# Performance work log

Hardware: AMD Instinct MI355X
Metric: run time of the kernel (lower is better)

The kernel has to match this reference:

```python
import jax, jax.numpy as jnp
import numpy as np

L_TAU = 0.8  # membrane leak/decay factor (l_tau in the torch module)
T, B, IN, H = 100, 256, 1024, 1024


def setup_inputs() -> dict:
    key = jax.random.key(0)
    k_x, k_w1, k_b1, k_w2, k_b2 = jax.random.split(key, 5)
    x = jax.random.normal(k_x, (T, B, IN), dtype=jnp.float32)
    W1 = jax.random.normal(k_w1, (H, IN), dtype=jnp.float32) / np.sqrt(IN)
    b1 = jax.random.normal(k_b1, (H,), dtype=jnp.float32) * 0.1 - 0.5
    W2 = jax.random.normal(k_w2, (H, H), dtype=jnp.float32) / np.sqrt(H)
    b2 = jax.random.normal(k_b2, (H,), dtype=jnp.float32) * 0.1 - 0.5
    return {"x": x, "W1": W1, "b1": b1, "W2": W2, "b2": b2}


def reference(x, W1, b1, W2, b2):
    """Two stacked SNU (spiking neural unit) layers scanned over T timesteps.

    Per layer (hard / non-soft SNU):
      u_t = W x_t + l_tau * s_{t-1} * (1 - y_{t-1})   # leaky membrane with reset-on-spike
      s_t = relu(u_t)                                  # membrane potential
      y_t = heaviside(s_t + b)                         # spike output
    Returns (spikes_l1 [T,B,H], mem_l1 [T,B,H], mem_l2 [T,B,H]) matching the
    torch forward's (spikes_, mem1_out, mem2_out).
    """
    dt = x.dtype
    Bsz = x.shape[1]
    H1 = W1.shape[0]
    H2 = W2.shape[0]

    def step(carry, x_t):
        s1, y1, s2, y2 = carry
        u1 = x_t @ W1.T + L_TAU * s1 * (1.0 - y1)     # [B, H1]
        s1n = jax.nn.relu(u1)
        y1n = (s1n + b1 > 0.0).astype(dt)
        u2 = y1n @ W2.T + L_TAU * s2 * (1.0 - y2)     # [B, H2]
        s2n = jax.nn.relu(u2)
        y2n = (s2n + b2 > 0.0).astype(dt)
        return (s1n, y1n, s2n, y2n), (y1n, s1n, s2n)

    init = (
        jnp.zeros((Bsz, H1), dt), jnp.zeros((Bsz, H1), dt),
        jnp.zeros((Bsz, H2), dt), jnp.zeros((Bsz, H2), dt),
    )
    _, (spikes, mem1, mem2) = jax.lax.scan(step, init, x)
    return spikes, mem1, mem2
```

## Files before the change

### kernel.cpp

```cpp
#include <hip/hip_runtime.h>


#define TILE 128
#define BK 32
#define NTILE (512 / BK)

typedef const __attribute__((address_space(1))) void* gptr_t;
typedef __attribute__((address_space(3))) void* sptr_t;

template<int ADD>
__global__ __launch_bounds__(256) void gemm_nt_swz(
    const float* __restrict__ A,
    const float* __restrict__ B,
    float* __restrict__ C,
    int N, int M, int K, int kbase)
{
#pragma clang fp contract(off)
    __shared__ float As[TILE * BK];
    __shared__ float Bs[TILE * BK];

    const int tid  = threadIdx.x;
    const int w    = tid >> 6;
    const int lane = tid & 63;
    const int tx   = lane & 7;
    const int ty   = lane >> 3;
    const int wr   = w >> 1;
    const int wc   = w & 1;
    const int row0 = wr * 64 + ty * 8;
    const int col0 = wc * 64 + tx * 8;

    const int n0 = blockIdx.x * TILE;
    const int m0 = blockIdx.y * TILE;

    const int lr8 = lane >> 3;
    const int lc  = lane & 7;

    float acc[8][8];
#pragma unroll
    for (int i = 0; i < 8; ++i)
#pragma unroll
        for (int j = 0; j < 8; ++j) acc[i][j] = 0.f;

    for (int kt = 0; kt < NTILE; ++kt) {
        const int k0 = kbase + kt * BK;
        __syncthreads();
#pragma unroll
        for (int is = 0; is < 4; ++is) {
            const int rb   = w * 4 + is;
            const int srow = rb * 8 + lr8;
            const int sc   = lc ^ (rb & 7);
            const float* ga = A + (size_t)(n0 + srow) * K + k0 + sc * 4;
            const float* gb = B + (size_t)(m0 + srow) * K + k0 + sc * 4;
            __builtin_amdgcn_global_load_lds((gptr_t)ga, (sptr_t)(As + rb * 8 * BK), 16, 0, 0);
            __builtin_amdgcn_global_load_lds((gptr_t)gb, (sptr_t)(Bs + rb * 8 * BK), 16, 0, 0);
        }
        __syncthreads();

#pragma unroll
        for (int c = 0; c < 8; ++c) {
            float4 bf[8];
#pragma unroll
            for (int j = 0; j < 8; ++j)
                bf[j] = *(const float4*)&Bs[(col0 + j) * BK + ((c ^ tx) << 2)];
#pragma unroll
            for (int i = 0; i < 8; ++i) {
                float4 af = *(const float4*)&As[(row0 + i) * BK + ((c ^ ty) << 2)];
#pragma unroll
                for (int j = 0; j < 8; ++j) {
                    acc[i][j] = __builtin_fmaf(af.x, bf[j].x, acc[i][j]);
                    acc[i][j] = __builtin_fmaf(af.y, bf[j].y, acc[i][j]);
                    acc[i][j] = __builtin_fmaf(af.z, bf[j].z, acc[i][j]);
                    acc[i][j] = __builtin_fmaf(af.w, bf[j].w, acc[i][j]);
                }
            }
        }
    }

#pragma unroll
    for (int i = 0; i < 8; ++i) {
        size_t row = (size_t)(n0 + row0 + i);
        float* Cp = C + row * M + m0 + col0;
        if (ADD) {
            float4 o0 = *(float4*)Cp;
            float4 o1 = *(float4*)(Cp + 4);
            o0.x = o0.x + acc[i][0]; o0.y = o0.y + acc[i][1];
            o0.z = o0.z + acc[i][2]; o0.w = o0.w + acc[i][3];
            o1.x = o1.x + acc[i][4]; o1.y = o1.y + acc[i][5];
            o1.z = o1.z + acc[i][6]; o1.w = o1.w + acc[i][7];
            *(float4*)Cp       = o0;
            *(float4*)(Cp + 4) = o1;
        } else {
            float4 o0 = {acc[i][0], acc[i][1], acc[i][2], acc[i][3]};
            float4 o1 = {acc[i][4], acc[i][5], acc[i][6], acc[i][7]};
            *(float4*)Cp       = o0;
            *(float4*)(Cp + 4) = o1;
        }
    }
}

__global__ __launch_bounds__(256) void scan_l1v(
    const float* __restrict__ Z, const float* __restrict__ bias,
    float* __restrict__ spikes, float* __restrict__ mem, int T, int BH)
{
#pragma clang fp contract(off)
    const int BH4 = BH >> 2;
    int i4 = blockIdx.x * blockDim.x + threadIdx.x;
    if (i4 >= BH4) return;
    const float4* Zv = (const float4*)Z;
    float4* spv  = (float4*)spikes;
    float4* memv = (float4*)mem;
    const float4 bb = *(const float4*)&bias[(i4 << 2) & 1023];

    float4 s = {0.f,0.f,0.f,0.f}, y = {0.f,0.f,0.f,0.f};
    float4 z = Zv[i4];
    for (int t = 0; t < T; ++t) {
        size_t idx = (size_t)t * BH4 + i4;
        float4 zn;
        if (t + 1 < T) zn = Zv[idx + BH4]; else zn = make_float4(0.f,0.f,0.f,0.f);
        float u;
        u = z.x + (0.8f * s.x) * (1.0f - y.x); s.x = fmaxf(u, 0.f); y.x = ((s.x + bb.x) > 0.f) ? 1.f : 0.f;
        u = z.y + (0.8f * s.y) * (1.0f - y.y); s.y = fmaxf(u, 0.f); y.y = ((s.y + bb.y) > 0.f) ? 1.f : 0.f;
        u = z.z + (0.8f * s.z) * (1.0f - y.z); s.z = fmaxf(u, 0.f); y.z = ((s.z + bb.z) > 0.f) ? 1.f : 0.f;
        u = z.w + (0.8f * s.w) * (1.0f - y.w); s.w = fmaxf(u, 0.f); y.w = ((s.w + bb.w) > 0.f) ? 1.f : 0.f;
        spv[idx]  = y;
        memv[idx] = s;
        z = zn;
    }
}

__global__ __launch_bounds__(256) void scan_l2v(
    float* __restrict__ Z, const float* __restrict__ bias, int T, int BH)
{
#pragma clang fp contract(off)
    const int BH4 = BH >> 2;
    int i4 = blockIdx.x * blockDim.x + threadIdx.x;
    if (i4 >= BH4) return;
    float4* Zv = (float4*)Z;
    const float4 bb = *(const float4*)&bias[(i4 << 2) & 1023];

    float4 s = {0.f,0.f,0.f,0.f}, y = {0.f,0.f,0.f,0.f};
    float4 z = Zv[i4];
    for (int t = 0; t < T; ++t) {
        size_t idx = (size_t)t * BH4 + i4;
        float4 zn;
        if (t + 1 < T) zn = Zv[idx + BH4]; else zn = make_float4(0.f,0.f,0.f,0.f);
        float u;
        u = z.x + (0.8f * s.x) * (1.0f - y.x); s.x = fmaxf(u, 0.f); y.x = ((s.x + bb.x) > 0.f) ? 1.f : 0.f;
        u = z.y + (0.8f * s.y) * (1.0f - y.y); s.y = fmaxf(u, 0.f); y.y = ((s.y + bb.y) > 0.f) ? 1.f : 0.f;
        u = z.z + (0.8f * s.z) * (1.0f - y.z); s.z = fmaxf(u, 0.f); y.z = ((s.z + bb.z) > 0.f) ? 1.f : 0.f;
        u = z.w + (0.8f * s.w) * (1.0f - y.w); s.w = fmaxf(u, 0.f); y.w = ((s.w + bb.w) > 0.f) ? 1.f : 0.f;
        Zv[idx] = s;
        z = zn;
    }
}

extern "C" void kernel_launch(void* const* d_in, const int* in_sizes, int n_in,
                              void* d_out, int out_size, void* d_ws, size_t ws_size,
                              hipStream_t stream)
{
    (void)in_sizes; (void)n_in; (void)out_size; (void)d_ws; (void)ws_size;

    const float* x  = (const float*)d_in[0];
    const float* W1 = (const float*)d_in[1];
    const float* b1 = (const float*)d_in[2];
    const float* W2 = (const float*)d_in[3];
    const float* b2 = (const float*)d_in[4];
    float* out = (float*)d_out;

    const int T = 100, Bsz = 256, IN = 1024, H = 1024;
    const int N  = T * Bsz;
    const int BH = Bsz * H;
    const size_t TBH = (size_t)T * BH;

    float* spikes = out;
    float* mem1   = out + TBH;
    float* zbuf   = out + 2 * TBH;

    dim3 ggrid(N / TILE, H / TILE);
    dim3 gblk(256);
    dim3 sgrid((BH / 4) / 256);
    dim3 sblk(256);

    gemm_nt_swz<0><<<ggrid, gblk, 0, stream>>>(x, W1, zbuf, N, H, IN, 0);
    gemm_nt_swz<1><<<ggrid, gblk, 0, stream>>>(x, W1, zbuf, N, H, IN, 512);
    scan_l1v<<<sgrid, sblk, 0, stream>>>(zbuf, b1, spikes, mem1, T, BH);
    gemm_nt_swz<0><<<ggrid, gblk, 0, stream>>>(spikes, W2, zbuf, N, H, H, 0);
    gemm_nt_swz<1><<<ggrid, gblk, 0, stream>>>(spikes, W2, zbuf, N, H, H, 512);
    scan_l2v<<<sgrid, sblk, 0, stream>>>(zbuf, b2, T, BH);
}
```

Measured before the change: 1.489 ms.

## Double-buffer GEMM LDS tiles and remap blocks for L2-friendly grouping

```diff
diff --git a/kernel.cpp b/kernel.cpp
--- a/kernel.cpp
+++ b/kernel.cpp
@@ -8,16 +8,53 @@
 typedef const __attribute__((address_space(1))) void* gptr_t;
 typedef __attribute__((address_space(3))) void* sptr_t;
 
+#define STAGE(ktv, AS, BS) do {                                               \
+    const int k0s = kbase + (ktv) * BK;                                       \
+    _Pragma("unroll")                                                         \
+    for (int is = 0; is < 4; ++is) {                                          \
+        const int rb   = w * 4 + is;                                          \
+        const int srow = rb * 8 + lr8;                                        \
+        const int sc   = lc ^ (rb & 7);                                       \
+        const float* ga = A + (size_t)(n0 + srow) * K + k0s + sc * 4;         \
+        const float* gb = B + (size_t)(m0 + srow) * K + k0s + sc * 4;         \
+        __builtin_amdgcn_global_load_lds((gptr_t)ga, (sptr_t)((AS) + rb * 8 * BK), 16, 0, 0); \
+        __builtin_amdgcn_global_load_lds((gptr_t)gb, (sptr_t)((BS) + rb * 8 * BK), 16, 0, 0); \
+    }                                                                         \
+} while (0)
+
+#define COMPUTE(AS, BS) do {                                                  \
+    _Pragma("unroll")                                                         \
+    for (int c = 0; c < 8; ++c) {                                             \
+        float4 bf[8];                                                         \
+        _Pragma("unroll")                                                     \
+        for (int j = 0; j < 8; ++j)                                           \
+            bf[j] = *(const float4*)&(BS)[(col0 + j) * BK + ((c ^ tx) << 2)]; \
+        _Pragma("unroll")                                                     \
+        for (int i = 0; i < 8; ++i) {                                         \
+            float4 af = *(const float4*)&(AS)[(row0 + i) * BK + ((c ^ ty) << 2)]; \
+            _Pragma("unroll")                                                 \
+            for (int j = 0; j < 8; ++j) {                                     \
+                acc[i][j] = __builtin_fmaf(af.x, bf[j].x, acc[i][j]);         \
+                acc[i][j] = __builtin_fmaf(af.y, bf[j].y, acc[i][j]);         \
+                acc[i][j] = __builtin_fmaf(af.z, bf[j].z, acc[i][j]);         \
+                acc[i][j] = __builtin_fmaf(af.w, bf[j].w, acc[i][j]);         \
+            }                                                                 \
+        }                                                                     \
+    }                                                                         \
+} while (0)
+
 template<int ADD>
-__global__ __launch_bounds__(256) void gemm_nt_swz(
+__global__ __launch_bounds__(256) void gemm_nt_db2(
     const float* __restrict__ A,
     const float* __restrict__ B,
     float* __restrict__ C,
     int N, int M, int K, int kbase)
 {
 #pragma clang fp contract(off)
-    __shared__ float As[TILE * BK];
-    __shared__ float Bs[TILE * BK];
+    __shared__ float As0[TILE * BK];
+    __shared__ float Bs0[TILE * BK];
+    __shared__ float As1[TILE * BK];
+    __shared__ float Bs1[TILE * BK];
 
     const int tid  = threadIdx.x;
     const int w    = tid >> 6;
@@ -29,8 +66,11 @@
     const int row0 = wr * 64 + ty * 8;
     const int col0 = wc * 64 + tx * 8;
 
-    const int n0 = blockIdx.x * TILE;
-    const int m0 = blockIdx.y * TILE;
+    const int id = blockIdx.x;
+    const int bx = (id & 7) | ((id >> 6) << 3);
+    const int by = (id >> 3) & 7;
+    const int n0 = bx * TILE;
+    const int m0 = by * TILE;
 
     const int lr8 = lane >> 3;
     const int lc  = lane & 7;
@@ -41,39 +81,16 @@
 #pragma unroll
         for (int j = 0; j < 8; ++j) acc[i][j] = 0.f;
 
-    for (int kt = 0; kt < NTILE; ++kt) {
-        const int k0 = kbase + kt * BK;
+    STAGE(0, As0, Bs0);
+    __syncthreads();
+
+    for (int kt = 0; kt < NTILE; kt += 2) {
+        if (kt + 1 < NTILE) STAGE(kt + 1, As1, Bs1);
+        COMPUTE(As0, Bs0);
         __syncthreads();
-#pragma unroll
-        for (int is = 0; is < 4; ++is) {
-            const int rb   = w * 4 + is;
-            const int srow = rb * 8 + lr8;
-            const int sc   = lc ^ (rb & 7);
-            const float* ga = A + (size_t)(n0 + srow) * K + k0 + sc * 4;
-            const float* gb = B + (size_t)(m0 + srow) * K + k0 + sc * 4;
-            __builtin_amdgcn_global_load_lds((gptr_t)ga, (sptr_t)(As + rb * 8 * BK), 16, 0, 0);
-            __builtin_amdgcn_global_load_lds((gptr_t)gb, (sptr_t)(Bs + rb * 8 * BK), 16, 0, 0);
-        }
+        if (kt + 2 < NTILE) STAGE(kt + 2, As0, Bs0);
+        COMPUTE(As1, Bs1);
         __syncthreads();
-
-#pragma unroll
-        for (int c = 0; c < 8; ++c) {
-            float4 bf[8];
-#pragma unroll
-            for (int j = 0; j < 8; ++j)
-                bf[j] = *(const float4*)&Bs[(col0 + j) * BK + ((c ^ tx) << 2)];
-#pragma unroll
-            for (int i = 0; i < 8; ++i) {
-                float4 af = *(const float4*)&As[(row0 + i) * BK + ((c ^ ty) << 2)];
-#pragma unroll
-                for (int j = 0; j < 8; ++j) {
-                    acc[i][j] = __builtin_fmaf(af.x, bf[j].x, acc[i][j]);
-                    acc[i][j] = __builtin_fmaf(af.y, bf[j].y, acc[i][j]);
-                    acc[i][j] = __builtin_fmaf(af.z, bf[j].z, acc[i][j]);
-                    acc[i][j] = __builtin_fmaf(af.w, bf[j].w, acc[i][j]);
-                }
-            }
-        }
     }
 
 #pragma unroll
@@ -176,15 +193,15 @@
     float* mem1   = out + TBH;
     float* zbuf   = out + 2 * TBH;
 
-    dim3 ggrid(N / TILE, H / TILE);
+    dim3 ggrid((N / TILE) * (H / TILE));
     dim3 gblk(256);
     dim3 sgrid((BH / 4) / 256);
     dim3 sblk(256);
 
-    gemm_nt_swz<0><<<ggrid, gblk, 0, stream>>>(x, W1, zbuf, N, H, IN, 0);
-    gemm_nt_swz<1><<<ggrid, gblk, 0, stream>>>(x, W1, zbuf, N, H, IN, 512);
+    gemm_nt_db2<0><<<ggrid, gblk, 0, stream>>>(x, W1, zbuf, N, H, IN, 0);
+    gemm_nt_db2<1><<<ggrid, gblk, 0, stream>>>(x, W1, zbuf, N, H, IN, 512);
     scan_l1v<<<sgrid, sblk, 0, stream>>>(zbuf, b1, spikes, mem1, T, BH);
-    gemm_nt_swz<0><<<ggrid, gblk, 0, stream>>>(spikes, W2, zbuf, N, H, H, 0);
-    gemm_nt_swz<1><<<ggrid, gblk, 0, stream>>>(spikes, W2, zbuf, N, H, H, 512);
+    gemm_nt_db2<0><<<ggrid, gblk, 0, stream>>>(spikes, W2, zbuf, N, H, H, 0);
+    gemm_nt_db2<1><<<ggrid, gblk, 0, stream>>>(spikes, W2, zbuf, N, H, H, 512);
     scan_l2v<<<sgrid, sblk, 0, stream>>>(zbuf, b2, T, BH);
 }
```

After: 5.648 ms. 279% more time.

## Fuse split-K halves into one launch writing separate buffers, sum in scans

Applied to the files above, without the earlier changes.

```diff
diff --git a/kernel.cpp b/kernel.cpp
--- a/kernel.cpp
+++ b/kernel.cpp
@@ -8,12 +8,13 @@
 typedef const __attribute__((address_space(1))) void* gptr_t;
 typedef __attribute__((address_space(3))) void* sptr_t;
 
-template<int ADD>
+template<int MODE, int SPLITK>
 __global__ __launch_bounds__(256) void gemm_nt_swz(
     const float* __restrict__ A,
     const float* __restrict__ B,
-    float* __restrict__ C,
-    int N, int M, int K, int kbase)
+    float* __restrict__ C0,
+    float* __restrict__ C1,
+    int N, int M, int K, int kbase_arg)
 {
 #pragma clang fp contract(off)
     __shared__ float As[TILE * BK];
@@ -29,8 +30,28 @@
     const int row0 = wr * 64 + ty * 8;
     const int col0 = wc * 64 + tx * 8;
 
-    const int n0 = blockIdx.x * TILE;
-    const int m0 = blockIdx.y * TILE;
+    int bx, by, kbase;
+    float* C;
+    if (SPLITK) {
+        const int id  = blockIdx.x;
+        const int xcd = id & 7;
+        const int s   = id >> 3;
+        const int r   = s & 15;
+        bx    = ((s >> 4) << 3) | xcd;
+        by    = r & 7;
+        kbase = (r >> 3) ? 512 : 0;
+        C     = (r >> 3) ? C1 : C0;
+    } else {
+        const int id  = blockIdx.x;
+        const int xcd = id & 7;
+        const int s   = id >> 3;
+        bx    = ((s >> 3) << 3) | xcd;
+        by    = s & 7;
+        kbase = kbase_arg;
+        C     = C0;
+    }
+    const int n0 = bx * TILE;
+    const int m0 = by * TILE;
 
     const int lr8 = lane >> 3;
     const int lc  = lane & 7;
@@ -80,7 +101,7 @@
     for (int i = 0; i < 8; ++i) {
         size_t row = (size_t)(n0 + row0 + i);
         float* Cp = C + row * M + m0 + col0;
-        if (ADD) {
+        if (MODE == 1) {
             float4 o0 = *(float4*)Cp;
             float4 o1 = *(float4*)(Cp + 4);
             o0.x = o0.x + acc[i][0]; o0.y = o0.y + acc[i][1];
@@ -98,25 +119,31 @@
     }
 }
 
+template<int HSUM>
 __global__ __launch_bounds__(256) void scan_l1v(
-    const float* __restrict__ Z, const float* __restrict__ bias,
+    const float* __restrict__ Z0, const float* __restrict__ Z1,
+    const float* __restrict__ bias,
     float* __restrict__ spikes, float* __restrict__ mem, int T, int BH)
 {
 #pragma clang fp contract(off)
     const int BH4 = BH >> 2;
     int i4 = blockIdx.x * blockDim.x + threadIdx.x;
     if (i4 >= BH4) return;
-    const float4* Zv = (const float4*)Z;
+    const float4* Zv0 = (const float4*)Z0;
+    const float4* Zv1 = (const float4*)Z1;
     float4* spv  = (float4*)spikes;
     float4* memv = (float4*)mem;
     const float4 bb = *(const float4*)&bias[(i4 << 2) & 1023];
 
     float4 s = {0.f,0.f,0.f,0.f}, y = {0.f,0.f,0.f,0.f};
-    float4 z = Zv[i4];
     for (int t = 0; t < T; ++t) {
         size_t idx = (size_t)t * BH4 + i4;
-        float4 zn;
-        if (t + 1 < T) zn = Zv[idx + BH4]; else zn = make_float4(0.f,0.f,0.f,0.f);
+        float4 z = Zv0[idx];
+        if (HSUM) {
+            float4 h1 = Zv1[idx];
+            z.x = z.x + h1.x; z.y = z.y + h1.y;
+            z.z = z.z + h1.z; z.w = z.w + h1.w;
+        }
         float u;
         u = z.x + (0.8f * s.x) * (1.0f - y.x); s.x = fmaxf(u, 0.f); y.x = ((s.x + bb.x) > 0.f) ? 1.f : 0.f;
         u = z.y + (0.8f * s.y) * (1.0f - y.y); s.y = fmaxf(u, 0.f); y.y = ((s.y + bb.y) > 0.f) ? 1.f : 0.f;
@@ -124,33 +151,37 @@
         u = z.w + (0.8f * s.w) * (1.0f - y.w); s.w = fmaxf(u, 0.f); y.w = ((s.w + bb.w) > 0.f) ? 1.f : 0.f;
         spv[idx]  = y;
         memv[idx] = s;
-        z = zn;
-    }
-}
-
+    }
+}
+
+template<int HSUM>
 __global__ __launch_bounds__(256) void scan_l2v(
-    float* __restrict__ Z, const float* __restrict__ bias, int T, int BH)
+    float* __restrict__ Z0, const float* __restrict__ Z1,
+    const float* __restrict__ bias, int T, int BH)
 {
 #pragma clang fp contract(off)
     const int BH4 = BH >> 2;
     int i4 = blockIdx.x * blockDim.x + threadIdx.x;
     if (i4 >= BH4) return;
-    float4* Zv = (float4*)Z;
+    float4* Zv0 = (float4*)Z0;
+    const float4* Zv1 = (const float4*)Z1;
     const float4 bb = *(const float4*)&bias[(i4 << 2) & 1023];
 
     float4 s = {0.f,0.f,0.f,0.f}, y = {0.f,0.f,0.f,0.f};
-    float4 z = Zv[i4];
     for (int t = 0; t < T; ++t) {
         size_t idx = (size_t)t * BH4 + i4;
-        float4 zn;
-        if (t + 1 < T) zn = Zv[idx + BH4]; else zn = make_float4(0.f,0.f,0.f,0.f);
+        float4 z = Zv0[idx];
+        if (HSUM) {
+            float4 h1 = Zv1[idx];
+            z.x = z.x + h1.x; z.y = z.y + h1.y;
+            z.z = z.z + h1.z; z.w = z.w + h1.w;
+        }
         float u;
         u = z.x + (0.8f * s.x) * (1.0f - y.x); s.x = fmaxf(u, 0.f); y.x = ((s.x + bb.x) > 0.f) ? 1.f : 0.f;
         u = z.y + (0.8f * s.y) * (1.0f - y.y); s.y = fmaxf(u, 0.f); y.y = ((s.y + bb.y) > 0.f) ? 1.f : 0.f;
         u = z.z + (0.8f * s.z) * (1.0f - y.z); s.z = fmaxf(u, 0.f); y.z = ((s.z + bb.z) > 0.f) ? 1.f : 0.f;
         u = z.w + (0.8f * s.w) * (1.0f - y.w); s.w = fmaxf(u, 0.f); y.w = ((s.w + bb.w) > 0.f) ? 1.f : 0.f;
-        Zv[idx] = s;
-        z = zn;
+        Zv0[idx] = s;
     }
 }
 
@@ -158,7 +189,7 @@
                               void* d_out, int out_size, void* d_ws, size_t ws_size,
                               hipStream_t stream)
 {
-    (void)in_sizes; (void)n_in; (void)out_size; (void)d_ws; (void)ws_size;
+    (void)in_sizes; (void)n_in; (void)out_size;
 
     const float* x  = (const float*)d_in[0];
     const float* W1 = (const float*)d_in[1];
@@ -176,15 +207,26 @@
     float* mem1   = out + TBH;
     float* zbuf   = out + 2 * TBH;
 
-    dim3 ggrid(N / TILE, H / TILE);
     dim3 gblk(256);
     dim3 sgrid((BH / 4) / 256);
     dim3 sblk(256);
 
-    gemm_nt_swz<0><<<ggrid, gblk, 0, stream>>>(x, W1, zbuf, N, H, IN, 0);
-    gemm_nt_swz<1><<<ggrid, gblk, 0, stream>>>(x, W1, zbuf, N, H, IN, 512);
-    scan_l1v<<<sgrid, sblk, 0, stream>>>(zbuf, b1, spikes, mem1, T, BH);
-    gemm_nt_swz<0><<<ggrid, gblk, 0, stream>>>(spikes, W2, zbuf, N, H, H, 0);
-    gemm_nt_swz<1><<<ggrid, gblk, 0, stream>>>(spikes, W2, zbuf, N, H, H, 512);
-    scan_l2v<<<sgrid, sblk, 0, stream>>>(zbuf, b2, T, BH);
-}
+    const bool hasws = ws_size >= TBH * sizeof(float);
+
+    if (hasws) {
+        float* zws = (float*)d_ws;
+        dim3 ggrid(3200);
+        gemm_nt_swz<0,1><<<ggrid, gblk, 0, stream>>>(x, W1, zbuf, zws, N, H, IN, 0);
+        scan_l1v<1><<<sgrid, sblk, 0, stream>>>(zbuf, zws, b1, spikes, mem1, T, BH);
+        gemm_nt_swz<0,1><<<ggrid, gblk, 0, stream>>>(spikes, W2, zbuf, zws, N, H, H, 0);
+        scan_l2v<1><<<sgrid, sblk, 0, stream>>>(zbuf, zws, b2, T, BH);
+    } else {
+        dim3 ggrid(1600);
+        gemm_nt_swz<0,0><<<ggrid, gblk, 0, stream>>>(x, W1, zbuf, nullptr, N, H, IN, 0);
+        gemm_nt_swz<1,0><<<ggrid, gblk, 0, stream>>>(x, W1, zbuf, nullptr, N, H, IN, 512);
+        scan_l1v<0><<<sgrid, sblk, 0, stream>>>(zbuf, nullptr, b1, spikes, mem1, T, BH);
+        gemm_nt_swz<0,0><<<ggrid, gblk, 0, stream>>>(spikes, W2, zbuf, nullptr, N, H, H, 0);
+        gemm_nt_swz<1,0><<<ggrid, gblk, 0, stream>>>(spikes, W2, zbuf, nullptr, N, H, H, 512);
+        scan_l2v<0><<<sgrid, sblk, 0, stream>>>(zbuf, nullptr, b2, T, BH);
+    }
+}
```

Result: faster. 1.412 ms (-5.2%).
